# Optimization experiments

Hardware: AMD Instinct MI355X
Metric: run time of the kernel (lower is better)

## Reference

```python
import jax, jax.numpy as jnp
import numpy as np

B, N, S, K, K2, C = 8, 131072, 1024, 64, 64, 32
RADIUS, RADIUS_POST = 0.4, 0.8
D1 = C + 6        # 38: mlp1 input (xyz + dim_box + feats)
H = 2 * C         # 64
D2 = H + 6        # 70: mlp2 input
H3 = 4 * H        # 256: mlp3 hidden


def _bgather(x, idx):
    # per-batch gather along axis 1 (points axis): x [B,N,...], idx [B,M] -> [B,M,...]
    return jax.vmap(lambda a, i: a[i])(x, idx)


def _conv_bn(x, w, s, t, relu=True):
    # 1x1 conv (matmul over channel) + folded eval-mode BN (scale/shift per channel)
    y = jnp.einsum('...c,cd->...d', x, w) * s + t
    return jnp.maximum(y, 0.0) if relu else y


def setup_inputs():
    key = jax.random.key(0)
    ks = jax.random.split(key, 20)
    inp = {
        'locs': jax.random.normal(ks[0], (B, N, 3), jnp.float32),
        'feats': jax.random.normal(ks[1], (B, C, N), jnp.float32),
        'boxes': jax.random.normal(ks[2], (B, N, 6), jnp.float32),
        'fps_inds': jax.random.randint(ks[3], (B, S), 0, N),
        'neighbor_inds': jax.random.randint(ks[4], (B, S * K), 0, N),
        'neighbor_inds2': jax.random.randint(ks[5], (B, S * K2), 0, S),
    }
    def w(k, i, o):
        return jax.random.normal(k, (i, o), jnp.float32) * (1.0 / np.sqrt(i))
    def bn(k, c):
        k1, k2 = jax.random.split(k)
        return (1.0 + 0.1 * jax.random.normal(k1, (c,), jnp.float32),
                0.1 * jax.random.normal(k2, (c,), jnp.float32))
    inp['w1a'] = w(ks[6], D1, C);  inp['s1a'], inp['t1a'] = bn(ks[7], C)
    inp['w1b'] = w(ks[8], C, H);   inp['s1b'], inp['t1b'] = bn(ks[9], H)
    inp['w2'] = w(ks[10], D2, H);  inp['s2'], inp['t2'] = bn(ks[11], H)
    inp['w3a'] = w(ks[12], H, H3); inp['s3a'], inp['t3a'] = bn(ks[13], H3)
    inp['w3b'] = w(ks[14], H3, H); inp['s3b'], inp['t3b'] = bn(ks[15], H)
    return inp


def reference(locs, feats, boxes, fps_inds, neighbor_inds, neighbor_inds2,
              w1a, s1a, t1a, w1b, s1b, t1b, w2, s2, t2,
              w3a, s3a, t3a, w3b, s3b, t3b):
    feats_nc = jnp.transpose(feats, (0, 2, 1))          # [B,N,C]
    dim_boxes = boxes[..., 3:] - boxes[..., :3]          # [B,N,3]

    fps_locs = _bgather(locs, fps_inds)                  # [B,S,3]
    fps_dim = _bgather(dim_boxes, fps_inds)              # [B,S,3]
    fps_boxes = _bgather(boxes, fps_inds)                # [B,S,6]

    # --- stage 1: ball-query gather on raw points ---
    gxyz = _bgather(locs, neighbor_inds).reshape(B, S, K, 3)
    gxyz = (gxyz - fps_locs[:, :, None, :]) / RADIUS
    gdim = _bgather(dim_boxes, neighbor_inds).reshape(B, S, K, 3)
    gdim = jnp.abs(gdim - fps_dim[:, :, None, :])
    gfeat = _bgather(feats_nc, neighbor_inds).reshape(B, S, K, C)
    g = jnp.concatenate([gxyz, gdim, gfeat], axis=-1)    # [B,S,K,38]

    h = _conv_bn(g, w1a, s1a, t1a, relu=True)
    h = _conv_bn(h, w1b, s1b, t1b, relu=True)            # [B,S,K,64]
    new_features = jnp.max(h, axis=2)                    # [B,S,64]
    identity = new_features

    # --- stage 2: ball-query gather on FPS points ---
    gxyz2 = _bgather(fps_locs, neighbor_inds2).reshape(B, S, K2, 3)
    gxyz2 = (gxyz2 - fps_locs[:, :, None, :]) / RADIUS_POST
    gdim2 = _bgather(fps_dim, neighbor_inds2).reshape(B, S, K2, 3)
    gdim2 = jnp.abs(gdim2 - fps_dim[:, :, None, :])
    gfeat2 = _bgather(new_features, neighbor_inds2).reshape(B, S, K2, H)
    g2 = jnp.concatenate([gxyz2, gdim2, gfeat2], axis=-1)  # [B,S,K2,70]

    h2 = _conv_bn(g2, w2, s2, t2, relu=False)            # [B,S,K2,64]
    h2 = jnp.max(h2, axis=2)                             # [B,S,64]

    # --- mlp_module3 (Conv1d bottleneck) + skip ---
    h3 = _conv_bn(h2, w3a, s3a, t3a, relu=True)          # [B,S,256]
    h3 = _conv_bn(h3, w3b, s3b, t3b, relu=False)         # [B,S,64]
    out = jnp.maximum(h3 + identity, 0.0)                # skip_act

    return fps_locs, jnp.transpose(out, (0, 2, 1)), fps_boxes, fps_inds
```

## Files before the change

kernel.cpp:

```cpp
#include <hip/hip_runtime.h>
#include <hip/hip_bf16.h>
#include <stdint.h>

#define DEV __device__ __forceinline__

constexpr int B_ = 8, N_ = 131072, S_ = 1024, C_ = 32;
constexpr float INV_R1 = 2.5f;
constexpr float INV_R2 = 1.25f;

constexpr int OW1AS = 0;
constexpr int OW1BS = 1216;
constexpr int OT1B  = 3264;
constexpr int OW2S  = 3328;
constexpr int OT2   = 7808;
constexpr int OW3AS = 7872;
constexpr int OT3A  = 24256;
constexpr int OW3BS = 24512;
constexpr int OT3B  = 40896;

constexpr size_t WS_CTR  = 163840;
constexpr size_t WS_NF   = WS_CTR  + (size_t)8192*104*4;
constexpr size_t WS_P2   = WS_NF   + (size_t)524288*4;
constexpr size_t WS_HOUT = WS_P2   + (size_t)524288*4;
constexpr size_t WS_PREC = WS_HOUT + (size_t)524288*4;

DEV float bfu(uint16_t u){ return __uint_as_float(((uint32_t)u) << 16); }

__global__ void k_weights(
    const float* __restrict__ w1a, const float* __restrict__ s1a,
    const float* __restrict__ w1b, const float* __restrict__ s1b,
    const float* __restrict__ t1b,
    const float* __restrict__ w2,  const float* __restrict__ s2,
    const float* __restrict__ t2,
    const float* __restrict__ w3a, const float* __restrict__ s3a,
    const float* __restrict__ t3a,
    const float* __restrict__ w3b, const float* __restrict__ s3b,
    const float* __restrict__ t3b,
    float* __restrict__ wsw)
{
  int t = blockIdx.x*256 + threadIdx.x;
  int nth = gridDim.x*256;
  for (int i=t;i<38*32;i+=nth)  wsw[OW1AS+i] = w1a[i]*s1a[i&31];
  for (int i=t;i<32*64;i+=nth)  wsw[OW1BS+i] = w1b[i]*s1b[i&63];
  for (int i=t;i<64;i+=nth)     wsw[OT1B+i]  = t1b[i];
  for (int i=t;i<70*64;i+=nth)  wsw[OW2S+i]  = w2[i]*s2[i&63];
  for (int i=t;i<64;i+=nth)     wsw[OT2+i]   = t2[i];
  for (int i=t;i<64*256;i+=nth) wsw[OW3AS+i] = w3a[i]*s3a[i&255];
  for (int i=t;i<256;i+=nth)    wsw[OT3A+i]  = t3a[i];
  for (int i=t;i<256*64;i+=nth) wsw[OW3BS+i] = w3b[i]*s3b[i&63];
  for (int i=t;i<64;i+=nth)     wsw[OT3B+i]  = t3b[i];
}

__global__ __launch_bounds__(256) void k_points(
    const float* __restrict__ locs,
    const float* __restrict__ feats,
    const float* __restrict__ wsw,
    __hip_bfloat16* __restrict__ prec)
{
  size_t p = (size_t)blockIdx.x*256 + threadIdx.x;
  int b = (int)(p >> 17);
  int pinb = (int)(p & (size_t)(N_-1));

  float x = locs[p*3+0]*INV_R1;
  float y = locs[p*3+1]*INV_R1;
  float z = locs[p*3+2]*INV_R1;

  float acc[32];
  #pragma unroll
  for (int j=0;j<32;j++)
    acc[j] = x*wsw[OW1AS+j] + y*wsw[OW1AS+32+j] + z*wsw[OW1AS+64+j];

  const float* fb = feats + (size_t)b*C_*N_ + pinb;
  float fcur[8], fnxt[8];
  #pragma unroll
  for (int i=0;i<8;i++) fcur[i] = fb[(size_t)i*N_];
  #pragma unroll
  for (int ch=0;ch<4;ch++){
    if (ch<3){
      #pragma unroll
      for (int i=0;i<8;i++) fnxt[i] = fb[(size_t)(8*(ch+1)+i)*N_];
    }
    #pragma unroll
    for (int i=0;i<8;i++){
      int c = 8*ch+i;
      #pragma unroll
      for (int j=0;j<32;j++)
        acc[j] = fmaf(fcur[i], wsw[OW1AS + (6+c)*32 + j], acc[j]);
    }
    #pragma unroll
    for (int i=0;i<8;i++) fcur[i] = fnxt[i];
  }
  union U { float4 v[4]; __hip_bfloat16 h[32]; } r;
  #pragma unroll
  for (int j=0;j<32;j++) r.h[j] = __float2bfloat16(acc[j]);
  float4* dst = (float4*)(prec + p*32);
  dst[0]=r.v[0]; dst[1]=r.v[1]; dst[2]=r.v[2]; dst[3]=r.v[3];
}

__global__ __launch_bounds__(256) void k_stage1c(
    const float* __restrict__ locs,
    const float* __restrict__ boxes,
    const int* __restrict__ fps_inds,
    const float* __restrict__ t1a,
    const int* __restrict__ ninds,
    const __hip_bfloat16* __restrict__ prec,
    const float* __restrict__ wsw,
    float* __restrict__ ctr,
    float* __restrict__ nf,
    float* __restrict__ p2,
    float* __restrict__ out0,
    float* __restrict__ out2,
    float* __restrict__ out3)
{
  int wid  = (blockIdx.x*256 + threadIdx.x) >> 6;
  int lane = threadIdx.x & 63;
  int uwid = __builtin_amdgcn_readfirstlane(wid);
  int b = uwid >> 10;

  int idx = fps_inds[uwid];
  size_t src = (size_t)b*N_ + (uint32_t)idx;
  float cx = locs[src*3+0], cy = locs[src*3+1], cz = locs[src*3+2];
  float bx0=boxes[src*6+0], bx1=boxes[src*6+1], bx2=boxes[src*6+2];
  float bx3=boxes[src*6+3], bx4=boxes[src*6+4], bx5=boxes[src*6+5];
  float d0=bx3-bx0, d1=bx4-bx1, d2=bx5-bx2;

  if (lane==0){
    out0[(size_t)uwid*3+0]=cx; out0[(size_t)uwid*3+1]=cy; out0[(size_t)uwid*3+2]=cz;
    out2[(size_t)uwid*6+0]=bx0; out2[(size_t)uwid*6+1]=bx1; out2[(size_t)uwid*6+2]=bx2;
    out2[(size_t)uwid*6+3]=bx3; out2[(size_t)uwid*6+4]=bx4; out2[(size_t)uwid*6+5]=bx5;
    out3[uwid] = (float)idx;
    ctr[(size_t)uwid*104+3]=d0; ctr[(size_t)uwid*104+4]=d1; ctr[(size_t)uwid*104+5]=d2;
  }
  {
    int j = lane & 31;
    float xr=cx*INV_R1, yr=cy*INV_R1, zr=cz*INV_R1;
    float c8 = t1a[j] - xr*wsw[OW1AS+j] - yr*wsw[OW1AS+32+j] - zr*wsw[OW1AS+64+j];
    float xq=cx*INV_R2, yq=cy*INV_R2, zq=cz*INV_R2;
    float q2l = wsw[OT2+lane] - xq*wsw[OW2S+lane] - yq*wsw[OW2S+64+lane] - zq*wsw[OW2S+128+lane];
    ctr[(size_t)uwid*104+40+lane] = q2l;

    int nbr = ninds[(size_t)uwid*64 + lane];
    size_t gp = (size_t)b*N_ + (uint32_t)nbr;

    union U { float4 v[4]; uint16_t u[32]; } r;
    const float4* psrc = (const float4*)(prec + gp*32);
    r.v[0]=psrc[0]; r.v[1]=psrc[1]; r.v[2]=psrc[2]; r.v[3]=psrc[3];

    const float2* bp = (const float2*)(boxes + gp*6);
    float2 q0=bp[0], q1=bp[1], q2=bp[2];

    float ad0=fabsf((q1.y-q0.x)-d0);
    float ad1=fabsf((q2.x-q0.y)-d1);
    float ad2=fabsf((q2.y-q1.x)-d2);

    float h[32];
    #pragma unroll
    for (int i=0;i<32;i++){
      float p = bfu(r.u[i]);
      float v = p + __shfl(c8, i) + ad0*wsw[OW1AS+96+i] + ad1*wsw[OW1AS+128+i] + ad2*wsw[OW1AS+160+i];
      h[i] = fmaxf(v, 0.f);
    }
    float acc[64];
    #pragma unroll
    for (int j2=0;j2<64;j2++) acc[j2] = wsw[OT1B+j2];
    #pragma unroll
    for (int i=0;i<32;i++){
      #pragma unroll
      for (int j2=0;j2<64;j2++)
        acc[j2] = fmaf(h[i], wsw[OW1BS + i*64 + j2], acc[j2]);
    }
    #pragma unroll
    for (int s=32;s>=1;s>>=1){
      bool up = (lane & s) != 0;
      #pragma unroll
      for (int i=0;i<s;i++){
        float lo = fmaxf(acc[i],   __shfl_xor(acc[i],   s));
        float hi = fmaxf(acc[s+i], __shfl_xor(acc[s+i], s));
        acc[i] = up ? hi : lo;
      }
    }
    float mine = fmaxf(acc[0], 0.f);
    nf[(size_t)uwid*64 + lane] = mine;

    float pv = (cx*INV_R2)*wsw[OW2S+lane]
             + (cy*INV_R2)*wsw[OW2S+64+lane]
             + (cz*INV_R2)*wsw[OW2S+128+lane];
    #pragma unroll
    for (int i=0;i<64;i++)
      pv = fmaf(__shfl(mine, i), wsw[OW2S + (6+i)*64 + lane], pv);
    p2[(size_t)uwid*64 + lane] = pv;
  }
}

__global__ __launch_bounds__(256) void k_stage23t(
    const int* __restrict__ ninds2,
    const float* __restrict__ wsw,
    const float* __restrict__ ctr,
    const float* __restrict__ nf,
    const float* __restrict__ p2,
    float* __restrict__ out1)
{
  int wid  = (blockIdx.x*256 + threadIdx.x) >> 6;
  int lane = threadIdx.x & 63;
  int uw = __builtin_amdgcn_readfirstlane(wid);
  int c0 = uw*4;
  int bS = c0 & ~1023;

  float q2v[4], m[4], cd0[4], cd1[4], cd2[4];
  #pragma unroll
  for (int g=0;g<4;g++){
    const float* cr = ctr + (size_t)(c0+g)*104;
    q2v[g] = cr[40+lane];
    cd0[g]=cr[3]; cd1[g]=cr[4]; cd2[g]=cr[5];
    m[g] = -3.4e38f;
  }
  float w30 = wsw[OW2S+192+lane];
  float w31 = wsw[OW2S+256+lane];
  float w32 = wsw[OW2S+320+lane];

  #pragma unroll 4
  for (int k=0;k<64;k++){
    #pragma unroll
    for (int g=0;g<4;g++){
      int nb = ninds2[(size_t)(c0+g)*64 + k];
      int gg = bS + nb;
      const float* ncr = ctr + (size_t)gg*104;
      float a0 = fabsf(ncr[3]-cd0[g]);
      float a1 = fabsf(ncr[4]-cd1[g]);
      float a2 = fabsf(ncr[5]-cd2[g]);
      float v = p2[(size_t)gg*64 + lane] + q2v[g] + a0*w30 + a1*w31 + a2*w32;
      m[g] = fmaxf(m[g], v);
    }
  }

  float h3[4][4];
  #pragma unroll
  for (int g=0;g<4;g++)
    #pragma unroll
    for (int t=0;t<4;t++) h3[g][t] = wsw[OT3A + t*64 + lane];
  #pragma unroll 8
  for (int i=0;i<64;i++){
    float wv0 = wsw[OW3AS + i*256 +   0 + lane];
    float wv1 = wsw[OW3AS + i*256 +  64 + lane];
    float wv2 = wsw[OW3AS + i*256 + 128 + lane];
    float wv3 = wsw[OW3AS + i*256 + 192 + lane];
    #pragma unroll
    for (int g=0;g<4;g++){
      float h2i = __shfl(m[g], i);
      h3[g][0] = fmaf(h2i, wv0, h3[g][0]);
      h3[g][1] = fmaf(h2i, wv1, h3[g][1]);
      h3[g][2] = fmaf(h2i, wv2, h3[g][2]);
      h3[g][3] = fmaf(h2i, wv3, h3[g][3]);
    }
  }
  #pragma unroll
  for (int g=0;g<4;g++)
    #pragma unroll
    for (int t=0;t<4;t++) h3[g][t] = fmaxf(h3[g][t], 0.f);

  float o[4];
  #pragma unroll
  for (int g=0;g<4;g++) o[g] = wsw[OT3B + lane];
  #pragma unroll
  for (int t=0;t<4;t++){
    #pragma unroll 8
    for (int l=0;l<64;l++){
      float wb = wsw[OW3BS + (t*64+l)*64 + lane];
      #pragma unroll
      for (int g=0;g<4;g++)
        o[g] = fmaf(__shfl(h3[g][t], l), wb, o[g]);
    }
  }
  float4 vals;
  float* vp = &vals.x;
  #pragma unroll
  for (int g=0;g<4;g++){
    float idv = nf[(size_t)(c0+g)*64 + lane];
    vp[g] = fmaxf(o[g] + idv, 0.f);
  }
  int b = c0 >> 10;
  int s = c0 & 1023;
  float4* dst = (float4*)(out1 + ((size_t)b*64 + lane)*S_ + s);
  *dst = vals;
}

extern "C" void kernel_launch(void* const* d_in, const int* in_sizes, int n_in,
                              void* d_out, int out_size, void* d_ws, size_t ws_size,
                              hipStream_t stream) {
  const float* locs  = (const float*)d_in[0];
  const float* feats = (const float*)d_in[1];
  const float* boxes = (const float*)d_in[2];
  const int* fps_inds = (const int*)d_in[3];
  const int* ninds    = (const int*)d_in[4];
  const int* ninds2   = (const int*)d_in[5];
  const float* w1a=(const float*)d_in[6];
  const float* s1a=(const float*)d_in[7];
  const float* t1a=(const float*)d_in[8];
  const float* w1b=(const float*)d_in[9];
  const float* s1b=(const float*)d_in[10];
  const float* t1b=(const float*)d_in[11];
  const float* w2 =(const float*)d_in[12];
  const float* s2 =(const float*)d_in[13];
  const float* t2 =(const float*)d_in[14];
  const float* w3a=(const float*)d_in[15];
  const float* s3a=(const float*)d_in[16];
  const float* t3a=(const float*)d_in[17];
  const float* w3b=(const float*)d_in[18];
  const float* s3b=(const float*)d_in[19];
  const float* t3b=(const float*)d_in[20];

  float* wsw  = (float*)d_ws;
  float* ctr  = (float*)((char*)d_ws + WS_CTR);
  float* nf   = (float*)((char*)d_ws + WS_NF);
  float* p2b  = (float*)((char*)d_ws + WS_P2);
  __hip_bfloat16* prec = (__hip_bfloat16*)((char*)d_ws + WS_PREC);

  float* out  = (float*)d_out;
  float* out0 = out;
  float* out1 = out + 24576;
  float* out2 = out + 548864;
  float* out3 = out + 598016;

  k_weights<<<160, 256, 0, stream>>>(w1a,s1a,w1b,s1b,t1b,w2,s2,t2,w3a,s3a,t3a,w3b,s3b,t3b,wsw);
  k_points<<<4096, 256, 0, stream>>>(locs, feats, wsw, prec);
  k_stage1c<<<2048, 256, 0, stream>>>(locs, boxes, fps_inds, t1a, ninds, prec, wsw, ctr, nf, p2b, out0, out2, out3);
  k_stage23t<<<512, 256, 0, stream>>>(ninds2, wsw, ctr, nf, p2b, out1);
}
```

Baseline: 398.2 us.

## Compute stage-1 second MLP layer with bf16 MFMA instead of scalar FMA

The 32x64 second conv of stage 1 is moved from a per-lane scalar FMA loop (64 accumulators per lane plus a shuffle max-reduction) onto MFMA 16x16x32 bf16 instructions. Hidden activations are converted to bf16 and staged through shared memory as A fragments. Pre-swizzled bf16 B fragments of the scaled w1b are built once in the weight kernel, and the max over neighbors is taken directly on the MFMA outputs. The aim is to cut VALU work and register pressure in this stage; the cost is bf16 rounding of the hidden activations and weights, plus an LDS round-trip and a block barrier.

```diff
diff --git a/kernel.cpp b/kernel.cpp
--- a/kernel.cpp
+++ b/kernel.cpp
@@ -23,8 +23,13 @@
 constexpr size_t WS_P2   = WS_NF   + (size_t)524288*4;
 constexpr size_t WS_HOUT = WS_P2   + (size_t)524288*4;
 constexpr size_t WS_PREC = WS_HOUT + (size_t)524288*4;
+constexpr size_t MiB = 1048576;
+constexpr size_t WS_BFRAG = 80*MiB;
 
 DEV float bfu(uint16_t u){ return __uint_as_float(((uint32_t)u) << 16); }
+
+typedef __attribute__((ext_vector_type(8))) short short8v;
+typedef __attribute__((ext_vector_type(4))) float float4v;
 
 __global__ void k_weights(
     const float* __restrict__ w1a, const float* __restrict__ s1a,
@@ -36,7 +41,8 @@
     const float* __restrict__ t3a,
     const float* __restrict__ w3b, const float* __restrict__ s3b,
     const float* __restrict__ t3b,
-    float* __restrict__ wsw)
+    float* __restrict__ wsw,
+    uint16_t* __restrict__ bfrag)
 {
   int t = blockIdx.x*256 + threadIdx.x;
   int nth = gridDim.x*256;
@@ -49,6 +55,13 @@
   for (int i=t;i<256;i+=nth)    wsw[OT3A+i]  = t3a[i];
   for (int i=t;i<256*64;i+=nth) wsw[OW3BS+i] = w3b[i]*s3b[i&63];
   for (int i=t;i<64;i+=nth)     wsw[OT3B+i]  = t3b[i];
+  for (int i=t;i<4*64*8;i+=nth){
+    int j = i & 7, l = (i>>3) & 63, ct = i >> 9;
+    int k = (l>>4)*8 + j;
+    int c = ct*16 + (l & 15);
+    __hip_bfloat16 v = __float2bfloat16(w1b[k*64 + c] * s1b[c]);
+    bfrag[i] = reinterpret_cast<uint16_t&>(v);
+  }
 }
 
 __global__ __launch_bounds__(256) void k_points(
@@ -97,7 +110,7 @@
   dst[0]=r.v[0]; dst[1]=r.v[1]; dst[2]=r.v[2]; dst[3]=r.v[3];
 }
 
-__global__ __launch_bounds__(256) void k_stage1c(
+__global__ __launch_bounds__(256, 4) void k_stage1m(
     const float* __restrict__ locs,
     const float* __restrict__ boxes,
     const int* __restrict__ fps_inds,
@@ -105,6 +118,7 @@
     const int* __restrict__ ninds,
     const __hip_bfloat16* __restrict__ prec,
     const float* __restrict__ wsw,
+    const uint16_t* __restrict__ bfrag,
     float* __restrict__ ctr,
     float* __restrict__ nf,
     float* __restrict__ p2,
@@ -112,10 +126,17 @@
     float* __restrict__ out2,
     float* __restrict__ out3)
 {
+  __shared__ alignas(16) uint16_t hsh[4][64][40];
   int wid  = (blockIdx.x*256 + threadIdx.x) >> 6;
   int lane = threadIdx.x & 63;
+  int wv   = threadIdx.x >> 6;
   int uwid = __builtin_amdgcn_readfirstlane(wid);
   int b = uwid >> 10;
+
+  short8v bfr[4];
+  #pragma unroll
+  for (int ct=0; ct<4; ct++)
+    bfr[ct] = *(const short8v*)(bfrag + ct*512 + lane*8);
 
   int idx = fps_inds[uwid];
   size_t src = (size_t)b*N_ + (uint32_t)idx;
@@ -131,65 +152,72 @@
     out3[uwid] = (float)idx;
     ctr[(size_t)uwid*104+3]=d0; ctr[(size_t)uwid*104+4]=d1; ctr[(size_t)uwid*104+5]=d2;
   }
-  {
-    int j = lane & 31;
-    float xr=cx*INV_R1, yr=cy*INV_R1, zr=cz*INV_R1;
-    float c8 = t1a[j] - xr*wsw[OW1AS+j] - yr*wsw[OW1AS+32+j] - zr*wsw[OW1AS+64+j];
-    float xq=cx*INV_R2, yq=cy*INV_R2, zq=cz*INV_R2;
-    float q2l = wsw[OT2+lane] - xq*wsw[OW2S+lane] - yq*wsw[OW2S+64+lane] - zq*wsw[OW2S+128+lane];
-    ctr[(size_t)uwid*104+40+lane] = q2l;
-
-    int nbr = ninds[(size_t)uwid*64 + lane];
-    size_t gp = (size_t)b*N_ + (uint32_t)nbr;
-
-    union U { float4 v[4]; uint16_t u[32]; } r;
-    const float4* psrc = (const float4*)(prec + gp*32);
-    r.v[0]=psrc[0]; r.v[1]=psrc[1]; r.v[2]=psrc[2]; r.v[3]=psrc[3];
-
-    const float2* bp = (const float2*)(boxes + gp*6);
-    float2 q0=bp[0], q1=bp[1], q2=bp[2];
-
-    float ad0=fabsf((q1.y-q0.x)-d0);
-    float ad1=fabsf((q2.x-q0.y)-d1);
-    float ad2=fabsf((q2.y-q1.x)-d2);
-
-    float h[32];
-    #pragma unroll
-    for (int i=0;i<32;i++){
-      float p = bfu(r.u[i]);
-      float v = p + __shfl(c8, i) + ad0*wsw[OW1AS+96+i] + ad1*wsw[OW1AS+128+i] + ad2*wsw[OW1AS+160+i];
-      h[i] = fmaxf(v, 0.f);
-    }
-    float acc[64];
-    #pragma unroll
-    for (int j2=0;j2<64;j2++) acc[j2] = wsw[OT1B+j2];
-    #pragma unroll
-    for (int i=0;i<32;i++){
-      #pragma unroll
-      for (int j2=0;j2<64;j2++)
-        acc[j2] = fmaf(h[i], wsw[OW1BS + i*64 + j2], acc[j2]);
-    }
-    #pragma unroll
-    for (int s=32;s>=1;s>>=1){
-      bool up = (lane & s) != 0;
-      #pragma unroll
-      for (int i=0;i<s;i++){
-        float lo = fmaxf(acc[i],   __shfl_xor(acc[i],   s));
-        float hi = fmaxf(acc[s+i], __shfl_xor(acc[s+i], s));
-        acc[i] = up ? hi : lo;
-      }
-    }
-    float mine = fmaxf(acc[0], 0.f);
-    nf[(size_t)uwid*64 + lane] = mine;
-
-    float pv = (cx*INV_R2)*wsw[OW2S+lane]
-             + (cy*INV_R2)*wsw[OW2S+64+lane]
-             + (cz*INV_R2)*wsw[OW2S+128+lane];
-    #pragma unroll
-    for (int i=0;i<64;i++)
-      pv = fmaf(__shfl(mine, i), wsw[OW2S + (6+i)*64 + lane], pv);
-    p2[(size_t)uwid*64 + lane] = pv;
-  }
+  int j = lane & 31;
+  float xr=cx*INV_R1, yr=cy*INV_R1, zr=cz*INV_R1;
+  float c8 = t1a[j] - xr*wsw[OW1AS+j] - yr*wsw[OW1AS+32+j] - zr*wsw[OW1AS+64+j];
+  float xq=cx*INV_R2, yq=cy*INV_R2, zq=cz*INV_R2;
+  float q2l = wsw[OT2+lane] - xq*wsw[OW2S+lane] - yq*wsw[OW2S+64+lane] - zq*wsw[OW2S+128+lane];
+  ctr[(size_t)uwid*104+40+lane] = q2l;
+
+  int nbr = ninds[(size_t)uwid*64 + lane];
+  size_t gp = (size_t)b*N_ + (uint32_t)nbr;
+
+  union U { float4 v[4]; uint16_t u[32]; } r;
+  const float4* psrc = (const float4*)(prec + gp*32);
+  r.v[0]=psrc[0]; r.v[1]=psrc[1]; r.v[2]=psrc[2]; r.v[3]=psrc[3];
+
+  const float2* bp = (const float2*)(boxes + gp*6);
+  float2 q0=bp[0], q1=bp[1], q2=bp[2];
+
+  float ad0=fabsf((q1.y-q0.x)-d0);
+  float ad1=fabsf((q2.x-q0.y)-d1);
+  float ad2=fabsf((q2.y-q1.x)-d2);
+
+  union HU { uint16_t u[32]; uint4 q[4]; } hu;
+  #pragma unroll
+  for (int i=0;i<32;i++){
+    float p = bfu(r.u[i]);
+    float v = p + __shfl(c8, i) + ad0*wsw[OW1AS+96+i] + ad1*wsw[OW1AS+128+i] + ad2*wsw[OW1AS+160+i];
+    __hip_bfloat16 hb = __float2bfloat16(fmaxf(v, 0.f));
+    hu.u[i] = reinterpret_cast<uint16_t&>(hb);
+  }
+  uint4* wp = (uint4*)&hsh[wv][lane][0];
+  wp[0]=hu.q[0]; wp[1]=hu.q[1]; wp[2]=hu.q[2]; wp[3]=hu.q[3];
+  __syncthreads();
+
+  int rbase = lane & 15;
+  int koff  = (lane >> 4) * 8;
+  short8v a[4];
+  #pragma unroll
+  for (int at=0; at<4; at++)
+    a[at] = *(const short8v*)&hsh[wv][at*16 + rbase][koff];
+
+  float4v zeroc = {0.f, 0.f, 0.f, 0.f};
+  float m0, m1, m2, m3;
+  #pragma unroll
+  for (int ct=0; ct<4; ct++){
+    float mm = -3.4e38f;
+    #pragma unroll
+    for (int at=0; at<4; at++){
+      float4v c = __builtin_amdgcn_mfma_f32_16x16x32_bf16(a[at], bfr[ct], zeroc, 0, 0, 0);
+      mm = fmaxf(mm, fmaxf(fmaxf(c[0], c[1]), fmaxf(c[2], c[3])));
+    }
+    mm = fmaxf(mm, __shfl_xor(mm, 16));
+    mm = fmaxf(mm, __shfl_xor(mm, 32));
+    if (ct==0) m0=mm; else if (ct==1) m1=mm; else if (ct==2) m2=mm; else m3=mm;
+  }
+  int g = lane >> 4;
+  float msel = g==0 ? m0 : (g==1 ? m1 : (g==2 ? m2 : m3));
+  float mine = fmaxf(msel + wsw[OT1B + lane], 0.f);
+  nf[(size_t)uwid*64 + lane] = mine;
+
+  float pv = (cx*INV_R2)*wsw[OW2S+lane]
+           + (cy*INV_R2)*wsw[OW2S+64+lane]
+           + (cz*INV_R2)*wsw[OW2S+128+lane];
+  #pragma unroll
+  for (int i=0;i<64;i++)
+    pv = fmaf(__shfl(mine, i), wsw[OW2S + (6+i)*64 + lane], pv);
+  p2[(size_t)uwid*64 + lane] = pv;
 }
 
 __global__ __launch_bounds__(256) void k_stage23t(
@@ -314,6 +342,7 @@
   float* nf   = (float*)((char*)d_ws + WS_NF);
   float* p2b  = (float*)((char*)d_ws + WS_P2);
   __hip_bfloat16* prec = (__hip_bfloat16*)((char*)d_ws + WS_PREC);
+  uint16_t* bfrag = (uint16_t*)((char*)d_ws + WS_BFRAG);
 
   float* out  = (float*)d_out;
   float* out0 = out;
@@ -321,8 +350,8 @@
   float* out2 = out + 548864;
   float* out3 = out + 598016;
 
-  k_weights<<<160, 256, 0, stream>>>(w1a,s1a,w1b,s1b,t1b,w2,s2,t2,w3a,s3a,t3a,w3b,s3b,t3b,wsw);
+  k_weights<<<160, 256, 0, stream>>>(w1a,s1a,w1b,s1b,t1b,w2,s2,t2,w3a,s3a,t3a,w3b,s3b,t3b,wsw,bfrag);
   k_points<<<4096, 256, 0, stream>>>(locs, feats, wsw, prec);
-  k_stage1c<<<2048, 256, 0, stream>>>(locs, boxes, fps_inds, t1a, ninds, prec, wsw, ctr, nf, p2b, out0, out2, out3);
+  k_stage1m<<<2048, 256, 0, stream>>>(locs, boxes, fps_inds, t1a, ninds, prec, wsw, bfrag, ctr, nf, p2b, out0, out2, out3);
   k_stage23t<<<512, 256, 0, stream>>>(ninds2, wsw, ctr, nf, p2b, out1);
 }
```

Measured after the change: 379.7 us. 4.6% less time.
